# Optimization experiments

Hardware: AMD Instinct MI355X
Metric: run time of the kernel (lower is better)

The kernel has to match this reference:

```python
import jax, jax.numpy as jnp
import numpy as np

LSP_ORDER = 32
RATE = 0.01
N_ITER = 4
MIN_D = RATE * np.pi / (LSP_ORDER + 1)  # _precompute


def setup_inputs() -> dict:
    key = jax.random.key(0)
    # LSP coefficients in radians, valid range (0, pi)
    w = jax.random.uniform(key, (256, 4096, LSP_ORDER + 1), dtype=jnp.float32,
                           minval=0.0, maxval=float(np.pi))
    return {"w": w}


def reference(w):
    min_d = jnp.asarray(MIN_D, w.dtype)
    pi = jnp.asarray(np.pi, w.dtype)
    K, w1 = w[..., :1], w[..., 1:]  # (..., 1), (..., M)

    def one_pass(w1):
        # Sequential left-to-right repair: each pair (m, m+1) is pushed apart
        # by half the deficit; the updated right element feeds the next step.
        wt = jnp.moveaxis(w1, -1, 0)  # (M, ...)

        def step(c, nxt):
            s = 0.5 * jnp.maximum(min_d - (nxt - c), 0.0)
            return nxt + s, c - s  # carry = updated w1[m+1], out = final w1[m]

        c_last, outs = jax.lax.scan(step, wt[0], wt[1:])
        w1n = jnp.concatenate([outs, c_last[None]], axis=0)  # (M, ...)
        return jnp.clip(jnp.moveaxis(w1n, 0, -1), min_d, pi - min_d)

    # Early-exit break in the original is a no-op once converged (step sizes
    # become 0 and clip is idempotent), so running all N_ITER is exact.
    for _ in range(N_ITER):
        w1 = one_pass(w1)

    return jnp.concatenate([K, w1], axis=-1)
```

## Files before the change

### kernel.cpp

```cpp
#include <hip/hip_runtime.h>
#include <math.h>


#define THREADS 64
#define ROW 33
#define TROWS 64
#define FPT (TROWS * ROW)
#define V4PT (FPT / 4)
#define GRID 2048

typedef const __attribute__((address_space(1))) unsigned int* gas_p;
typedef __attribute__((address_space(3))) unsigned int* las_p;

__device__ __forceinline__ void stage_tile(const float* __restrict__ gin,
                                           las_p s, int tid)
{
    gas_p g = (gas_p)gin;
#pragma unroll
    for (int j = 0; j < 8; ++j)
        __builtin_amdgcn_global_load_lds(g + (size_t)(tid + j * THREADS) * 4,
                                         s + (size_t)(tid + j * THREADS) * 4,
                                         16, 0, 0);
    if (tid < (V4PT - 8 * THREADS))
        __builtin_amdgcn_global_load_lds(g + (size_t)(tid + 8 * THREADS) * 4,
                                         s + (size_t)(tid + 8 * THREADS) * 4,
                                         16, 0, 0);
}

__global__ __launch_bounds__(THREADS) void lsp_stability_kernel(
    const float* __restrict__ in, float* __restrict__ out, int tiles)
{
    __shared__ alignas(16) float smem[2][FPT];
    const int tid = threadIdx.x;
    const int bid = blockIdx.x;
    if (bid >= tiles) return;
    const int grid = (int)gridDim.x;
    const int nt = (tiles - bid + grid - 1) / grid;

    const float MIND = (float)(0.01 * M_PI / 33.0);
    const float PI_F = (float)M_PI;
    const float HI = PI_F - MIND;

    stage_tile(in + (size_t)bid * FPT, (las_p)&smem[0][0], tid);

    for (int t = 0; t < nt; ++t) {
        const size_t tile = (size_t)bid + (size_t)t * grid;
        const int cur = t & 1;

        if (t + 1 < nt)
            stage_tile(in + (tile + grid) * FPT, (las_p)&smem[cur ^ 1][0], tid);

        if (t > 0 && t + 1 < nt)
            asm volatile("s_waitcnt vmcnt(18)" ::: "memory");
        else if (t == 0 && t + 1 == nt)
            asm volatile("s_waitcnt vmcnt(0)" ::: "memory");
        else
            asm volatile("s_waitcnt vmcnt(9)" ::: "memory");

        float w[32];
        float* row = &smem[cur][0] + tid * ROW;
#pragma unroll
        for (int k = 0; k < 32; ++k) w[k] = row[k + 1];

#pragma unroll
        for (int it = 0; it < 4; ++it) {
            float c = w[0];
#pragma unroll
            for (int k = 1; k < 32; ++k) {
                float nxt = w[k];
                float sft = 0.5f * fmaxf(MIND - (nxt - c), 0.0f);
                w[k - 1] = c - sft;
                c = nxt + sft;
            }
            w[31] = c;
#pragma unroll
            for (int k = 0; k < 32; ++k)
                w[k] = fminf(fmaxf(w[k], MIND), HI);
        }

#pragma unroll
        for (int k = 0; k < 32; ++k) row[k + 1] = w[k];

        float4* out4 = (float4*)(out + tile * FPT);
        const float4* s4 = (const float4*)&smem[cur][0];
#pragma unroll
        for (int j = 0; j < 8; ++j)
            out4[tid + j * THREADS] = s4[tid + j * THREADS];
        if (tid < (V4PT - 8 * THREADS))
            out4[tid + 8 * THREADS] = s4[tid + 8 * THREADS];
    }
}

extern "C" void kernel_launch(void* const* d_in, const int* in_sizes, int n_in,
                              void* d_out, int out_size, void* d_ws, size_t ws_size,
                              hipStream_t stream) {
    const float* in = (const float*)d_in[0];
    float* out = (float*)d_out;
    const int tiles = in_sizes[0] / FPT;
    const int blocks = tiles < GRID ? tiles : GRID;
    lsp_stability_kernel<<<blocks, THREADS, 0, stream>>>(in, out, tiles);
}
```

Before: 238.5 us.

## Replace async global-to-LDS double buffer with register-prefetch single buffer

Measured after the change: 263.9 us. 1.11x slower.

```diff
diff --git a/kernel.cpp b/kernel.cpp
--- a/kernel.cpp
+++ b/kernel.cpp
@@ -7,30 +7,13 @@
 #define TROWS 64
 #define FPT (TROWS * ROW)
 #define V4PT (FPT / 4)
-#define GRID 2048
-
-typedef const __attribute__((address_space(1))) unsigned int* gas_p;
-typedef __attribute__((address_space(3))) unsigned int* las_p;
-
-__device__ __forceinline__ void stage_tile(const float* __restrict__ gin,
-                                           las_p s, int tid)
-{
-    gas_p g = (gas_p)gin;
-#pragma unroll
-    for (int j = 0; j < 8; ++j)
-        __builtin_amdgcn_global_load_lds(g + (size_t)(tid + j * THREADS) * 4,
-                                         s + (size_t)(tid + j * THREADS) * 4,
-                                         16, 0, 0);
-    if (tid < (V4PT - 8 * THREADS))
-        __builtin_amdgcn_global_load_lds(g + (size_t)(tid + 8 * THREADS) * 4,
-                                         s + (size_t)(tid + 8 * THREADS) * 4,
-                                         16, 0, 0);
-}
+#define TAIL (V4PT - 8 * THREADS)
+#define GRID 4096
 
 __global__ __launch_bounds__(THREADS) void lsp_stability_kernel(
     const float* __restrict__ in, float* __restrict__ out, int tiles)
 {
-    __shared__ alignas(16) float smem[2][FPT];
+    __shared__ alignas(16) float smem[FPT];
     const int tid = threadIdx.x;
     const int bid = blockIdx.x;
     if (bid >= tiles) return;
@@ -41,24 +24,32 @@
     const float PI_F = (float)M_PI;
     const float HI = PI_F - MIND;
 
-    stage_tile(in + (size_t)bid * FPT, (las_p)&smem[0][0], tid);
+    float4* s4 = (float4*)smem;
+    float4 r[9];
+
+    {
+        const float4* g4 = (const float4*)(in + (size_t)bid * FPT);
+#pragma unroll
+        for (int j = 0; j < 8; ++j) r[j] = g4[tid + j * THREADS];
+        if (tid < TAIL) r[8] = g4[tid + 8 * THREADS];
+    }
 
     for (int t = 0; t < nt; ++t) {
         const size_t tile = (size_t)bid + (size_t)t * grid;
-        const int cur = t & 1;
 
-        if (t + 1 < nt)
-            stage_tile(in + (tile + grid) * FPT, (las_p)&smem[cur ^ 1][0], tid);
+#pragma unroll
+        for (int j = 0; j < 8; ++j) s4[tid + j * THREADS] = r[j];
+        if (tid < TAIL) s4[tid + 8 * THREADS] = r[8];
 
-        if (t > 0 && t + 1 < nt)
-            asm volatile("s_waitcnt vmcnt(18)" ::: "memory");
-        else if (t == 0 && t + 1 == nt)
-            asm volatile("s_waitcnt vmcnt(0)" ::: "memory");
-        else
-            asm volatile("s_waitcnt vmcnt(9)" ::: "memory");
+        if (t + 1 < nt) {
+            const float4* g4 = (const float4*)(in + (tile + grid) * FPT);
+#pragma unroll
+            for (int j = 0; j < 8; ++j) r[j] = g4[tid + j * THREADS];
+            if (tid < TAIL) r[8] = g4[tid + 8 * THREADS];
+        }
 
         float w[32];
-        float* row = &smem[cur][0] + tid * ROW;
+        float* row = smem + tid * ROW;
 #pragma unroll
         for (int k = 0; k < 32; ++k) w[k] = row[k + 1];
 
@@ -82,11 +73,10 @@
         for (int k = 0; k < 32; ++k) row[k + 1] = w[k];
 
         float4* out4 = (float4*)(out + tile * FPT);
-        const float4* s4 = (const float4*)&smem[cur][0];
 #pragma unroll
         for (int j = 0; j < 8; ++j)
             out4[tid + j * THREADS] = s4[tid + j * THREADS];
-        if (tid < (V4PT - 8 * THREADS))
+        if (tid < TAIL)
             out4[tid + 8 * THREADS] = s4[tid + 8 * THREADS];
     }
 }
```
